# Performance work log

Hardware: AMD Instinct MI355X
Metric: run time of the kernel (lower is better)

## Reference

```python
import jax, jax.numpy as jnp
import numpy as np

DIM = 256
CODEBOOK_SIZE = 1024
CODEBOOK_DIM = 1024
COMMITMENT_COST = 1.0
CODEBOOK_COST = 0.25
LN_EPS = 1e-5


def setup_inputs() -> dict:
    key = jax.random.key(0)
    ks = jax.random.split(key, 6)
    x = jax.random.normal(ks[0], (4, 8192, DIM), dtype=jnp.float32)
    ln_gamma = jnp.ones((DIM,), jnp.float32)
    ln_beta = jnp.zeros((DIM,), jnp.float32)
    # pre_proj Linear(dim -> codebook_dim), stored as (in, out)
    pre_w = jax.random.normal(ks[1], (DIM, CODEBOOK_DIM), jnp.float32) / np.sqrt(DIM)
    pre_b = jnp.zeros((CODEBOOK_DIM,), jnp.float32)
    # codebook: unit-norm rows scaled by sqrt(codebook_dim)
    e = jax.random.normal(ks[2], (CODEBOOK_SIZE, CODEBOOK_DIM), jnp.float32)
    embed = e / jnp.linalg.norm(e, axis=1, keepdims=True) * np.sqrt(CODEBOOK_DIM)
    # post_proj Linear(codebook_dim -> dim)
    post_w = jax.random.normal(ks[3], (CODEBOOK_DIM, DIM), jnp.float32) / np.sqrt(CODEBOOK_DIM)
    post_b = jnp.zeros((DIM,), jnp.float32)
    return {"x": x, "ln_gamma": ln_gamma, "ln_beta": ln_beta,
            "pre_w": pre_w, "pre_b": pre_b, "embed": embed,
            "post_w": post_w, "post_b": post_b}


def _layer_norm(x, g, b):
    mu = jnp.mean(x, axis=-1, keepdims=True)
    var = jnp.mean(jnp.square(x - mu), axis=-1, keepdims=True)
    return (x - mu) * jax.lax.rsqrt(var + LN_EPS) * g + b


def reference(x, ln_gamma, ln_beta, pre_w, pre_b, embed, post_w, post_b):
    B, N, D = x.shape
    sg = jax.lax.stop_gradient
    # pre_norm -> GELU -> pre_proj
    x_normed = _layer_norm(x, ln_gamma, ln_beta)
    z_e = jax.nn.gelu(x_normed, approximate=False) @ pre_w + pre_b  # (B,N,Dc)
    flat = z_e.reshape(-1, CODEBOOK_DIM)  # (BN, Dc)
    # squared L2 distances to codebook: ||z||^2 - 2 z.E^T + ||e||^2
    z_sq = jnp.sum(flat * flat, axis=1, keepdims=True)        # (BN,1)
    e_sq = jnp.sum(embed * embed, axis=1)                      # (K,)
    dist = z_sq - 2.0 * (flat @ embed.T) + e_sq[None, :]       # (BN,K)
    indices = jnp.argmin(dist, axis=1)                          # (BN,)
    z_q = embed[indices]                                        # (BN,Dc)
    # losses
    codebook_loss = CODEBOOK_COST * jnp.mean(jnp.square(sg(flat) - z_q))
    commitment_loss = COMMITMENT_COST * jnp.mean(jnp.square(flat - sg(z_q)))
    vq_loss = codebook_loss + commitment_loss
    # straight-through estimator + post projection
    z_q_st = flat + sg(z_q - flat)
    quantized = (z_q_st.reshape(B, N, CODEBOOK_DIM)) @ post_w + post_b  # (B,N,D)
    return quantized, indices.reshape(B, N), vq_loss
```

## Files before the change

### kernel.cpp

```cpp
#include <hip/hip_runtime.h>
#include <math.h>

typedef __attribute__((ext_vector_type(8))) short short8;
typedef __attribute__((ext_vector_type(4))) float f32x4;

__device__ __forceinline__ unsigned short f2bf(float f) {
  unsigned u = __float_as_uint(f);
  unsigned r = (u + 0x7FFFu + ((u >> 16) & 1u)) >> 16;
  return (unsigned short)r;
}

__device__ __forceinline__ void gload_lds16(const void* gsrc, void* ldst) {
  __builtin_amdgcn_global_load_lds(
      (__attribute__((address_space(1))) void*)(void*)(size_t)(const char*)gsrc,
      (__attribute__((address_space(3))) void*)ldst, 16, 0, 0);
}

__global__ __launch_bounds__(256) void wtrans_kernel(
    const float* __restrict__ pre_w, float* __restrict__ wtf) {
  __shared__ float tile[64][65];
  const int bc = blockIdx.x;
  const int bd = blockIdx.y;
  const int t = threadIdx.x;
  const int col = t & 63, rr = t >> 6;
#pragma unroll
  for (int i = 0; i < 16; ++i) {
    int row = rr + i * 4;
    tile[row][col] = pre_w[(size_t)(bd * 64 + row) * 1024 + bc * 64 + col];
  }
  __syncthreads();
#pragma unroll
  for (int i = 0; i < 16; ++i) {
    int row = rr + i * 4;
    wtf[(size_t)(bc * 64 + row) * 256 + bd * 64 + col] = tile[col][row];
  }
}

__global__ __launch_bounds__(256) void esq_kernel(
    const float* __restrict__ embed, const float* __restrict__ pre_b,
    float* __restrict__ e_sq, float* __restrict__ qv, float* __restrict__ c0) {
  int t = threadIdx.x, l = t & 63, w = t >> 6;
  int k = blockIdx.x * 4 + w;
  const float* er = embed + (size_t)k * 1024;
  float s1 = 0.f, s2 = 0.f;
#pragma unroll
  for (int j = 0; j < 16; ++j) {
    float e = er[l + 64 * j];
    s1 += e * e;
    s2 += pre_b[l + 64 * j] * e;
  }
  for (int m = 32; m; m >>= 1) { s1 += __shfl_xor(s1, m); s2 += __shfl_xor(s2, m); }
  if (l == 0) { e_sq[k] = s1; qv[k] = s2; c0[k] = s1 - 2.0f * s2 - 1024.0f; }
}

__global__ __launch_bounds__(512) void pgemm_kernel(
    const float* __restrict__ embed, const float* __restrict__ wtf,
    float* __restrict__ prow, unsigned short* __restrict__ prowbf) {
  __shared__ float Es[4][1024];
  __shared__ double Pd[4][1024];
  const int t = threadIdx.x;
  const int k0 = blockIdx.x * 4;
  *(float4*)(&Es[0][0] + t * 8) = *(const float4*)(embed + (size_t)k0 * 1024 + t * 8);
  *(float4*)(&Es[0][0] + t * 8 + 4) = *(const float4*)(embed + (size_t)k0 * 1024 + t * 8 + 4);
  __syncthreads();
  const int sl = t >> 6;
  const int jg = t & 63;
  const int cbase = sl * 128;
  double a[4][4] = {};
  const float* wp = wtf + (size_t)cbase * 256 + jg * 4;
#pragma unroll 8
  for (int cc = 0; cc < 128; ++cc) {
    float4 w4 = *(const float4*)(wp + (size_t)cc * 256);
    int c = cbase + cc;
#pragma unroll
    for (int kk = 0; kk < 4; ++kk) {
      double e = (double)Es[kk][c];
      a[kk][0] += (double)w4.x * e;
      a[kk][1] += (double)w4.y * e;
      a[kk][2] += (double)w4.z * e;
      a[kk][3] += (double)w4.w * e;
    }
  }
  if (sl >= 4)
#pragma unroll
    for (int kk = 0; kk < 4; ++kk)
#pragma unroll
      for (int x = 0; x < 4; ++x) Pd[sl - 4][kk * 256 + jg * 4 + x] = a[kk][x];
  __syncthreads();
  if (sl < 4)
#pragma unroll
    for (int kk = 0; kk < 4; ++kk)
#pragma unroll
      for (int x = 0; x < 4; ++x) a[kk][x] += Pd[sl][kk * 256 + jg * 4 + x];
  __syncthreads();
  if (sl >= 2 && sl < 4)
#pragma unroll
    for (int kk = 0; kk < 4; ++kk)
#pragma unroll
      for (int x = 0; x < 4; ++x) Pd[sl - 2][kk * 256 + jg * 4 + x] = a[kk][x];
  __syncthreads();
  if (sl < 2)
#pragma unroll
    for (int kk = 0; kk < 4; ++kk)
#pragma unroll
      for (int x = 0; x < 4; ++x) a[kk][x] += Pd[sl][kk * 256 + jg * 4 + x];
  __syncthreads();
  if (sl == 1)
#pragma unroll
    for (int kk = 0; kk < 4; ++kk)
#pragma unroll
      for (int x = 0; x < 4; ++x) Pd[0][kk * 256 + jg * 4 + x] = a[kk][x];
  __syncthreads();
  if (sl == 0) {
#pragma unroll
    for (int kk = 0; kk < 4; ++kk) {
      float4 o;
      o.x = (float)(a[kk][0] + Pd[0][kk * 256 + jg * 4 + 0]);
      o.y = (float)(a[kk][1] + Pd[0][kk * 256 + jg * 4 + 1]);
      o.z = (float)(a[kk][2] + Pd[0][kk * 256 + jg * 4 + 2]);
      o.w = (float)(a[kk][3] + Pd[0][kk * 256 + jg * 4 + 3]);
      *(float4*)(prow + (size_t)(k0 + kk) * 256 + jg * 4) = o;
      ushort4 u;
      u.x = f2bf(o.x); u.y = f2bf(o.y); u.z = f2bf(o.z); u.w = f2bf(o.w);
      *(ushort4*)(prowbf + (size_t)(k0 + kk) * 256 + jg * 4) = u;
    }
  }
}

__global__ __launch_bounds__(512) void eproj_kernel(
    const float* __restrict__ embed, const float* __restrict__ post_w,
    const float* __restrict__ post_b, float* __restrict__ eproj) {
  __shared__ float Es[4][1024];
  __shared__ float Ps[8][1024];
  const int t = threadIdx.x;
  const int k0 = blockIdx.x * 4;
  *(float4*)(&Es[0][0] + t * 8) = *(const float4*)(embed + (size_t)k0 * 1024 + t * 8);
  *(float4*)(&Es[0][0] + t * 8 + 4) = *(const float4*)(embed + (size_t)k0 * 1024 + t * 8 + 4);
  __syncthreads();
  const int sl = t >> 6, jg = t & 63;
  const int dbase = sl * 128;
  float4 a[4] = {};
  const float* wp = post_w + (size_t)dbase * 256 + jg * 4;
#pragma unroll 8
  for (int dd = 0; dd < 128; ++dd) {
    float4 w4 = *(const float4*)(wp + (size_t)dd * 256);
    int d = dbase + dd;
#pragma unroll
    for (int kk = 0; kk < 4; ++kk) {
      float e = Es[kk][d];
      a[kk].x += w4.x * e; a[kk].y += w4.y * e;
      a[kk].z += w4.z * e; a[kk].w += w4.w * e;
    }
  }
#pragma unroll
  for (int kk = 0; kk < 4; ++kk)
    *(float4*)(&Ps[sl][kk * 256 + jg * 4]) = a[kk];
  __syncthreads();
#pragma unroll
  for (int rep = 0; rep < 2; ++rep) {
    int o = t + rep * 512;
    float s = Ps[0][o] + Ps[1][o] + Ps[2][o] + Ps[3][o] +
              Ps[4][o] + Ps[5][o] + Ps[6][o] + Ps[7][o];
    int kk = o >> 8, j = o & 255;
    eproj[(size_t)(k0 + kk) * 256 + j] = s + post_b[j];
  }
}

__global__ __launch_bounds__(512) void qmat_kernel(
    const float* __restrict__ pre_w, const float* __restrict__ wtf,
    const float* __restrict__ pre_b,
    unsigned short* __restrict__ qbf, float* __restrict__ wbv) {
  __shared__ float Es[4][1024];
  __shared__ float Ps[8][1024];
  const int t = threadIdx.x;
  const int sl = t >> 6, jg = t & 63;
  if (blockIdx.x < 64) {
    const int a0i = blockIdx.x * 4;
    *(float4*)(&Es[0][0] + t * 8) = *(const float4*)(pre_w + (size_t)a0i * 1024 + t * 8);
    *(float4*)(&Es[0][0] + t * 8 + 4) = *(const float4*)(pre_w + (size_t)a0i * 1024 + t * 8 + 4);
    __syncthreads();
    const int cbase = sl * 128;
    float4 a[4] = {};
    const float* wp = wtf + (size_t)cbase * 256 + jg * 4;
#pragma unroll 8
    for (int cc = 0; cc < 128; ++cc) {
      float4 w4 = *(const float4*)(wp + (size_t)cc * 256);
      int c = cbase + cc;
#pragma unroll
      for (int kk = 0; kk < 4; ++kk) {
        float e = Es[kk][c];
        a[kk].x += w4.x * e; a[kk].y += w4.y * e;
        a[kk].z += w4.z * e; a[kk].w += w4.w * e;
      }
    }
#pragma unroll
    for (int kk = 0; kk < 4; ++kk)
      *(float4*)(&Ps[sl][kk * 256 + jg * 4]) = a[kk];
    __syncthreads();
#pragma unroll
    for (int rep = 0; rep < 2; ++rep) {
      int o = t + rep * 512;
      float s = Ps[0][o] + Ps[1][o] + Ps[2][o] + Ps[3][o] +
                Ps[4][o] + Ps[5][o] + Ps[6][o] + Ps[7][o];
      int kk = o >> 8, j = o & 255;
      qbf[(size_t)(a0i + kk) * 256 + j] = f2bf(s);
    }
  } else {
    const int cbase = sl * 128;
    float4 a = {0.f, 0.f, 0.f, 0.f};
    const float* wp = wtf + (size_t)cbase * 256 + jg * 4;
#pragma unroll 8
    for (int cc = 0; cc < 128; ++cc) {
      float4 w4 = *(const float4*)(wp + (size_t)cc * 256);
      float b = pre_b[cbase + cc];
      a.x += w4.x * b; a.y += w4.y * b; a.z += w4.z * b; a.w += w4.w * b;
    }
    *(float4*)(&Ps[sl][jg * 4]) = a;
    float sb = 0.f;
    if (t < 256) {
      float4 bv = *(const float4*)(pre_b + t * 4);
      sb = bv.x * bv.x + bv.y * bv.y + bv.z * bv.z + bv.w * bv.w;
    }
    for (int m = 32; m; m >>= 1) sb += __shfl_xor(sb, m);
    if ((t & 63) == 0 && t < 256) Es[0][t >> 6] = sb;
    __syncthreads();
    if (t < 256) {
      float s = Ps[0][t] + Ps[1][t] + Ps[2][t] + Ps[3][t] +
                Ps[4][t] + Ps[5][t] + Ps[6][t] + Ps[7][t];
      wbv[t] = 2.f * s;
    }
    if (t == 0) wbv[256] = Es[0][0] + Es[0][1] + Es[0][2] + Es[0][3];
  }
}

__global__ __launch_bounds__(256) void lngelu_kernel(
    const float* __restrict__ x, const float* __restrict__ gamma,
    const float* __restrict__ beta, float* __restrict__ g,
    unsigned short* __restrict__ gbf) {
  int t = threadIdx.x, l = t & 63, w = t >> 6;
  int r = blockIdx.x * 4 + w;
  const float4 xv = *(const float4*)(x + (size_t)r * 256 + l * 4);
  float s = xv.x + xv.y + xv.z + xv.w;
  for (int m = 32; m; m >>= 1) s += __shfl_xor(s, m);
  const float mu = s * (1.0f / 256.0f);
  float dx = xv.x - mu, dy = xv.y - mu, dz = xv.z - mu, dw = xv.w - mu;
  float vs = dx * dx + dy * dy + dz * dz + dw * dw;
  for (int m = 32; m; m >>= 1) vs += __shfl_xor(vs, m);
  const float rstd = rsqrtf(vs * (1.0f / 256.0f) + 1e-5f);
  float4 gm = *(const float4*)(gamma + l * 4);
  float4 bt = *(const float4*)(beta + l * 4);
  float v0 = dx * rstd * gm.x + bt.x;
  float v1 = dy * rstd * gm.y + bt.y;
  float v2 = dz * rstd * gm.z + bt.z;
  float v3 = dw * rstd * gm.w + bt.w;
  const float is2 = 0.70710678118654752f;
  float4 o;
  o.x = 0.5f * v0 * (1.0f + erff(v0 * is2));
  o.y = 0.5f * v1 * (1.0f + erff(v1 * is2));
  o.z = 0.5f * v2 * (1.0f + erff(v2 * is2));
  o.w = 0.5f * v3 * (1.0f + erff(v3 * is2));
  *(float4*)(g + (size_t)r * 256 + l * 4) = o;
  ushort4 u;
  u.x = f2bf(o.x); u.y = f2bf(o.y); u.z = f2bf(o.z); u.w = f2bf(o.w);
  *(ushort4*)(gbf + (size_t)r * 256 + l * 4) = u;
}

__device__ __forceinline__ void stage_tile256(
    int t, const unsigned short* __restrict__ Asrc, size_t a_row_stride,
    const unsigned short* __restrict__ Bsrc, size_t b_row_stride, int k0,
    unsigned short* Ab, unsigned short* Bb) {
#pragma unroll
  for (int i = 0; i < 4; ++i) {
    int ca = t + 256 * i;
    int r = ca >> 3;
    int sp = (ca & 7) ^ (r & 7);
    gload_lds16(Asrc + (size_t)r * a_row_stride + k0 + sp * 8, (char*)Ab + ca * 16);
    gload_lds16(Bsrc + (size_t)r * b_row_stride + k0 + sp * 8, (char*)Bb + ca * 16);
  }
}

#define SAFE_LOOP_BODY(cur)                                                    \
    const unsigned short* Ab = &lds[cur][0];                                   \
    const unsigned short* Bb = &lds[cur][8192];                                \
    _Pragma("unroll")                                                          \
    for (int ks = 0; ks < 2; ++ks) {                                           \
      const int sp = ((ks << 2) + (l >> 4)) ^ (l & 7);                         \
      short8 af[4], bq[4];                                                     \
      _Pragma("unroll")                                                        \
      for (int mi = 0; mi < 4; ++mi)                                           \
        af[mi] = *(const short8*)(Ab + (wm + mi * 16 + (l & 15)) * 64 + sp * 8); \
      _Pragma("unroll")                                                        \
      for (int ni = 0; ni < 4; ++ni)                                           \
        bq[ni] = *(const short8*)(Bb + (wn + ni * 16 + (l & 15)) * 64 + sp * 8); \
      _Pragma("unroll")                                                        \
      for (int mi = 0; mi < 4; ++mi)                                           \
        _Pragma("unroll")                                                      \
        for (int ni = 0; ni < 4; ++ni)                                         \
          acc[mi][ni] = __builtin_amdgcn_mfma_f32_16x16x32_bf16(af[mi], bq[ni], acc[mi][ni], 0, 0, 0); \
    }

__global__ __launch_bounds__(256) void g1_kernel(
    const unsigned short* __restrict__ gbf,
    const unsigned short* __restrict__ prowbf,
    const float* __restrict__ c0,
    unsigned short* __restrict__ scores) {
  __shared__ unsigned short lds[2][16384];
  const int t = threadIdx.x;
  const int bn = blockIdx.x;
  const int bm = blockIdx.y;
  const int m0 = bm * 128;
  const unsigned short* Bsrc = prowbf + bn * 128 * 256;
  f32x4 acc[4][4] = {};
  const int w = t >> 6, l = t & 63;
  const int wm = (w >> 1) * 64, wn = (w & 1) * 64;

  stage_tile256(t, gbf + (size_t)m0 * 256, 256, Bsrc, 256, 0, &lds[0][0], &lds[0][8192]);
  __syncthreads();
  for (int kt = 0; kt < 4; ++kt) {
    const int cur = kt & 1;
    if (kt < 3)
      stage_tile256(t, gbf + (size_t)m0 * 256, 256, Bsrc, 256, (kt + 1) * 64,
                    &lds[cur ^ 1][0], &lds[cur ^ 1][8192]);
    SAFE_LOOP_BODY(cur)
    __syncthreads();
  }
  const int lrow = (l >> 4) * 4;
  const int lcol = l & 15;
  const int n0 = bn * 128;
#pragma unroll
  for (int mi = 0; mi < 4; ++mi)
#pragma unroll
    for (int ni = 0; ni < 4; ++ni) {
      int gcol = n0 + wn + ni * 16 + lcol;
      float cc = c0[gcol];
#pragma unroll
      for (int r = 0; r < 4; ++r) {
        int grow = m0 + wm + mi * 16 + lrow + r;
        scores[(size_t)grow * 1024 + gcol] = f2bf(cc - 2.0f * acc[mi][ni][r]);
      }
    }
}

__global__ __launch_bounds__(256) void zq_kernel(
    const unsigned short* __restrict__ gbf, const unsigned short* __restrict__ qbf,
    const float* __restrict__ g, const float* __restrict__ wbv,
    float* __restrict__ z_sq) {
  __shared__ unsigned short lds[2][16384];
  const int t = threadIdx.x;
  const int bn = blockIdx.x;
  const int bm = blockIdx.y;
  const int m0 = bm * 128;
  const unsigned short* Bsrc = qbf + bn * 128 * 256;
  f32x4 acc[4][4] = {};
  const int w = t >> 6, l = t & 63;
  const int wm = (w >> 1) * 64, wn = (w & 1) * 64;

  stage_tile256(t, gbf + (size_t)m0 * 256, 256, Bsrc, 256, 0, &lds[0][0], &lds[0][8192]);
  __syncthreads();
  for (int kt = 0; kt < 4; ++kt) {
    const int cur = kt & 1;
    if (kt < 3)
      stage_tile256(t, gbf + (size_t)m0 * 256, 256, Bsrc, 256, (kt + 1) * 64,
                    &lds[cur ^ 1][0], &lds[cur ^ 1][8192]);
    SAFE_LOOP_BODY(cur)
    __syncthreads();
  }
  const int lrow = (l >> 4) * 4;
  const int lcol = l & 15;
  const float bsq = wbv[256];
#pragma unroll
  for (int mi = 0; mi < 4; ++mi)
#pragma unroll
    for (int r = 0; r < 4; ++r) {
      int grow = m0 + wm + mi * 16 + lrow + r;
      float v = 0.f;
#pragma unroll
      for (int ni = 0; ni < 4; ++ni) {
        int gcol = bn * 128 + wn + ni * 16 + lcol;
        float gv = g[(size_t)grow * 256 + gcol];
        v += gv * (acc[mi][ni][r] + wbv[gcol]);
      }
      v += __shfl_xor(v, 1); v += __shfl_xor(v, 2);
      v += __shfl_xor(v, 4); v += __shfl_xor(v, 8);
      if (lcol == 0)
        atomicAdd(&z_sq[grow], v + ((bn == 0 && wn == 0) ? bsq : 0.f));
    }
}

__global__ __launch_bounds__(256) void refine_kernel(
    const unsigned short* __restrict__ scores, const float* __restrict__ g,
    const float* __restrict__ prow, const float* __restrict__ e_sq,
    const float* __restrict__ qv, const float* __restrict__ z_sq,
    const float* __restrict__ eproj, float* __restrict__ out_q,
    float* __restrict__ fidx, float* __restrict__ loss_slots) {
  const int t = threadIdx.x, l = t & 63, w = t >> 6;
  const int r = blockIdx.x * 4 + w;
  const unsigned short* srow = scores + (size_t)r * 1024;
  uint4 q0 = *(const uint4*)(srow + l * 16);
  uint4 q1 = *(const uint4*)(srow + l * 16 + 8);
  float f[16];
  {
    unsigned uu[8] = {q0.x, q0.y, q0.z, q0.w, q1.x, q1.y, q1.z, q1.w};
#pragma unroll
    for (int j = 0; j < 8; ++j) {
      f[2 * j] = __uint_as_float(uu[j] << 16);
      f[2 * j + 1] = __uint_as_float(uu[j] & 0xFFFF0000u);
    }
  }
  float mn = f[0];
#pragma unroll
  for (int j = 1; j < 16; ++j) mn = fminf(mn, f[j]);
  for (int m = 32; m; m >>= 1) mn = fminf(mn, __shfl_xor(mn, m));
  const float T = mn + 8.0f;

  float gv[4];
  const float* gr = g + (size_t)r * 256;
#pragma unroll
  for (int j = 0; j < 4; ++j) gv[j] = gr[l + 64 * j];

  float bestd = 1e30f; int bestk = 0x7fffffff;
#pragma unroll 1
  for (int j = 0; j < 16; ++j) {
    unsigned long long msk = __ballot(f[j] <= T);
    while (msk) {
      int src = __ffsll(msk) - 1;
      msk &= msk - 1;
      int k = src * 16 + j;
      const float* pr = prow + (size_t)k * 256;
      float p = 0.f;
#pragma unroll
      for (int jj = 0; jj < 4; ++jj) p += gv[jj] * pr[l + 64 * jj];
      for (int m = 32; m; m >>= 1) p += __shfl_xor(p, m);
      float d = e_sq[k] - 2.0f * (p + qv[k]);
      if (d < bestd || (d == bestd && k < bestk)) { bestd = d; bestk = k; }
    }
  }
  if (l == 0) {
    fidx[r] = (float)bestk;
    atomicAdd(&loss_slots[r & 2047], z_sq[r] + bestd);
  }
  float4 o = *(const float4*)(eproj + (size_t)bestk * 256 + l * 4);
  *(float4*)(out_q + (size_t)r * 256 + l * 4) = o;
}

__global__ __launch_bounds__(256) void loss_final_kernel(
    const float* __restrict__ slots, float* __restrict__ out_loss) {
  float s = 0.f;
  for (int i = threadIdx.x; i < 2048; i += 256) s += slots[i];
  for (int m = 32; m; m >>= 1) s += __shfl_xor(s, m);
  __shared__ float ws_[4];
  if ((threadIdx.x & 63) == 0) ws_[threadIdx.x >> 6] = s;
  __syncthreads();
  if (threadIdx.x == 0)
    out_loss[0] = 1.25f * (ws_[0] + ws_[1] + ws_[2] + ws_[3]) / 33554432.0f;
}

extern "C" void kernel_launch(void* const* d_in, const int* in_sizes, int n_in,
                              void* d_out, int out_size, void* d_ws, size_t ws_size,
                              hipStream_t stream) {
  const float* x = (const float*)d_in[0];
  const float* ln_g = (const float*)d_in[1];
  const float* ln_b = (const float*)d_in[2];
  const float* pre_w = (const float*)d_in[3];
  const float* pre_b = (const float*)d_in[4];
  const float* embed = (const float*)d_in[5];
  const float* post_w = (const float*)d_in[6];
  const float* post_b = (const float*)d_in[7];
  float* out_q = (float*)d_out;
  float* out_idx = out_q + 8388608;
  float* out_loss = out_q + 8421376;

  char* ws = (char*)d_ws;
  size_t off = 0;
  auto alloc = [&](size_t n) { char* p = ws + off; off += (n + 255) & ~(size_t)255; return p; };
  float* g_f32 = (float*)alloc(33554432);
  unsigned short* g_bf = (unsigned short*)alloc(16777216);
  unsigned short* scores = (unsigned short*)alloc(67108864);
  float* prow = (float*)alloc(1048576);
  unsigned short* prowbf = (unsigned short*)alloc(524288);
  unsigned short* qbf = (unsigned short*)alloc(131072);
  float* wtf = (float*)alloc(1048576);
  float* eproj = (float*)alloc(1048576);
  float* wbv = (float*)alloc(2048);
  float* e_sq = (float*)alloc(4096);
  float* qv = (float*)alloc(4096);
  float* c0 = (float*)alloc(4096);
  float* z_sq = (float*)alloc(131072);
  float* slots = (float*)alloc(8192);
  (void)ws_size; (void)in_sizes; (void)n_in; (void)out_size;

  hipMemsetAsync(z_sq, 0, 131072, stream);
  hipMemsetAsync(slots, 0, 8192, stream);

  dim3 wtg(16, 4);
  wtrans_kernel<<<wtg, 256, 0, stream>>>(pre_w, wtf);
  esq_kernel<<<256, 256, 0, stream>>>(embed, pre_b, e_sq, qv, c0);
  pgemm_kernel<<<256, 512, 0, stream>>>(embed, wtf, prow, prowbf);
  eproj_kernel<<<256, 512, 0, stream>>>(embed, post_w, post_b, eproj);
  qmat_kernel<<<65, 512, 0, stream>>>(pre_w, wtf, pre_b, qbf, wbv);
  lngelu_kernel<<<8192, 256, 0, stream>>>(x, ln_g, ln_b, g_f32, g_bf);
  dim3 g1grid(8, 256);
  g1_kernel<<<g1grid, 256, 0, stream>>>(g_bf, prowbf, c0, scores);
  dim3 zqgrid(2, 256);
  zq_kernel<<<zqgrid, 256, 0, stream>>>(g_bf, qbf, g_f32, wbv, z_sq);
  refine_kernel<<<8192, 256, 0, stream>>>(scores, g_f32, prow, e_sq, qv, z_sq,
                                          eproj, out_q, out_idx, slots);
  loss_final_kernel<<<1, 256, 0, stream>>>(slots, out_loss);
}
```

Baseline: 164.6 us.

## Merge six prep kernels into two block-dispatched kernels and swap GEMM grid axes

The transpose, e_sq, eproj and LayerNorm+GELU kernels are folded into one launch that picks its role from the block index, and pgemm and qmat are folded into a second launch. This cuts the number of small launches and the gaps between them, and lets independent prep work run concurrently. The g1 and zq grids now put the M dimension on blockIdx.x, which changes block scheduling order and so L2 reuse of the B operand. The cost is larger 48KB shared-memory reservations and 512-thread blocks for the light paths, which may lower occupancy for the LayerNorm blocks.

New measurement: 148.9 us. 1.11x faster.

```diff
diff --git a/kernel.cpp b/kernel.cpp
--- a/kernel.cpp
+++ b/kernel.cpp
@@ -16,166 +16,190 @@
       (__attribute__((address_space(3))) void*)ldst, 16, 0, 0);
 }
 
-__global__ __launch_bounds__(256) void wtrans_kernel(
-    const float* __restrict__ pre_w, float* __restrict__ wtf) {
-  __shared__ float tile[64][65];
-  const int bc = blockIdx.x;
-  const int bd = blockIdx.y;
+__global__ __launch_bounds__(512) void prep1_kernel(
+    const float* __restrict__ x, const float* __restrict__ ln_g,
+    const float* __restrict__ ln_b, const float* __restrict__ pre_w,
+    const float* __restrict__ pre_b, const float* __restrict__ embed,
+    const float* __restrict__ post_w, const float* __restrict__ post_b,
+    float* __restrict__ g, unsigned short* __restrict__ gbf,
+    float* __restrict__ wtf, float* __restrict__ e_sq,
+    float* __restrict__ qv, float* __restrict__ c0,
+    float* __restrict__ eproj) {
+  __shared__ __align__(16) char smem[49152];
+  const int blk = blockIdx.x;
   const int t = threadIdx.x;
-  const int col = t & 63, rr = t >> 6;
-#pragma unroll
-  for (int i = 0; i < 16; ++i) {
-    int row = rr + i * 4;
-    tile[row][col] = pre_w[(size_t)(bd * 64 + row) * 1024 + bc * 64 + col];
-  }
-  __syncthreads();
-#pragma unroll
-  for (int i = 0; i < 16; ++i) {
-    int row = rr + i * 4;
-    wtf[(size_t)(bc * 64 + row) * 256 + bd * 64 + col] = tile[col][row];
-  }
-}
-
-__global__ __launch_bounds__(256) void esq_kernel(
-    const float* __restrict__ embed, const float* __restrict__ pre_b,
-    float* __restrict__ e_sq, float* __restrict__ qv, float* __restrict__ c0) {
-  int t = threadIdx.x, l = t & 63, w = t >> 6;
-  int k = blockIdx.x * 4 + w;
-  const float* er = embed + (size_t)k * 1024;
-  float s1 = 0.f, s2 = 0.f;
-#pragma unroll
-  for (int j = 0; j < 16; ++j) {
-    float e = er[l + 64 * j];
-    s1 += e * e;
-    s2 += pre_b[l + 64 * j] * e;
-  }
-  for (int m = 32; m; m >>= 1) { s1 += __shfl_xor(s1, m); s2 += __shfl_xor(s2, m); }
-  if (l == 0) { e_sq[k] = s1; qv[k] = s2; c0[k] = s1 - 2.0f * s2 - 1024.0f; }
-}
-
-__global__ __launch_bounds__(512) void pgemm_kernel(
-    const float* __restrict__ embed, const float* __restrict__ wtf,
-    float* __restrict__ prow, unsigned short* __restrict__ prowbf) {
-  __shared__ float Es[4][1024];
-  __shared__ double Pd[4][1024];
-  const int t = threadIdx.x;
-  const int k0 = blockIdx.x * 4;
-  *(float4*)(&Es[0][0] + t * 8) = *(const float4*)(embed + (size_t)k0 * 1024 + t * 8);
-  *(float4*)(&Es[0][0] + t * 8 + 4) = *(const float4*)(embed + (size_t)k0 * 1024 + t * 8 + 4);
-  __syncthreads();
-  const int sl = t >> 6;
-  const int jg = t & 63;
-  const int cbase = sl * 128;
-  double a[4][4] = {};
-  const float* wp = wtf + (size_t)cbase * 256 + jg * 4;
+  if (blk < 4096) {
+    const int l = t & 63, w = t >> 6;
+    const int r = blk * 8 + w;
+    const float4 xv = *(const float4*)(x + (size_t)r * 256 + l * 4);
+    float s = xv.x + xv.y + xv.z + xv.w;
+    for (int m = 32; m; m >>= 1) s += __shfl_xor(s, m);
+    const float mu = s * (1.0f / 256.0f);
+    float dx = xv.x - mu, dy = xv.y - mu, dz = xv.z - mu, dw = xv.w - mu;
+    float vs = dx * dx + dy * dy + dz * dz + dw * dw;
+    for (int m = 32; m; m >>= 1) vs += __shfl_xor(vs, m);
+    const float rstd = rsqrtf(vs * (1.0f / 256.0f) + 1e-5f);
+    float4 gm = *(const float4*)(ln_g + l * 4);
+    float4 bt = *(const float4*)(ln_b + l * 4);
+    float v0 = dx * rstd * gm.x + bt.x;
+    float v1 = dy * rstd * gm.y + bt.y;
+    float v2 = dz * rstd * gm.z + bt.z;
+    float v3 = dw * rstd * gm.w + bt.w;
+    const float is2 = 0.70710678118654752f;
+    float4 o;
+    o.x = 0.5f * v0 * (1.0f + erff(v0 * is2));
+    o.y = 0.5f * v1 * (1.0f + erff(v1 * is2));
+    o.z = 0.5f * v2 * (1.0f + erff(v2 * is2));
+    o.w = 0.5f * v3 * (1.0f + erff(v3 * is2));
+    *(float4*)(g + (size_t)r * 256 + l * 4) = o;
+    ushort4 u;
+    u.x = f2bf(o.x); u.y = f2bf(o.y); u.z = f2bf(o.z); u.w = f2bf(o.w);
+    *(ushort4*)(gbf + (size_t)r * 256 + l * 4) = u;
+  } else if (blk < 4160) {
+    float (*tile)[65] = (float(*)[65])smem;
+    const int b = blk - 4096;
+    const int bc = b & 15, bd = b >> 4;
+    const int col = t & 63, rr = t >> 6;
+#pragma unroll
+    for (int i = 0; i < 8; ++i) {
+      int row = rr + i * 8;
+      tile[row][col] = pre_w[(size_t)(bd * 64 + row) * 1024 + bc * 64 + col];
+    }
+    __syncthreads();
+#pragma unroll
+    for (int i = 0; i < 8; ++i) {
+      int row = rr + i * 8;
+      wtf[(size_t)(bc * 64 + row) * 256 + bd * 64 + col] = tile[col][row];
+    }
+  } else if (blk < 4416) {
+    float (*Es)[1024] = (float(*)[1024])smem;
+    float (*Ps)[1024] = (float(*)[1024])(smem + 16384);
+    const int k0 = (blk - 4160) * 4;
+    *(float4*)(&Es[0][0] + t * 8) = *(const float4*)(embed + (size_t)k0 * 1024 + t * 8);
+    *(float4*)(&Es[0][0] + t * 8 + 4) = *(const float4*)(embed + (size_t)k0 * 1024 + t * 8 + 4);
+    __syncthreads();
+    const int sl = t >> 6, jg = t & 63;
+    const int dbase = sl * 128;
+    float4 a[4] = {};
+    const float* wp = post_w + (size_t)dbase * 256 + jg * 4;
 #pragma unroll 8
-  for (int cc = 0; cc < 128; ++cc) {
-    float4 w4 = *(const float4*)(wp + (size_t)cc * 256);
-    int c = cbase + cc;
-#pragma unroll
-    for (int kk = 0; kk < 4; ++kk) {
-      double e = (double)Es[kk][c];
-      a[kk][0] += (double)w4.x * e;
-      a[kk][1] += (double)w4.y * e;
-      a[kk][2] += (double)w4.z * e;
-      a[kk][3] += (double)w4.w * e;
-    }
-  }
-  if (sl >= 4)
+    for (int dd = 0; dd < 128; ++dd) {
+      float4 w4 = *(const float4*)(wp + (size_t)dd * 256);
+      int d = dbase + dd;
+#pragma unroll
+      for (int kk = 0; kk < 4; ++kk) {
+        float e = Es[kk][d];
+        a[kk].x += w4.x * e; a[kk].y += w4.y * e;
+        a[kk].z += w4.z * e; a[kk].w += w4.w * e;
+      }
+    }
 #pragma unroll
     for (int kk = 0; kk < 4; ++kk)
-#pragma unroll
-      for (int x = 0; x < 4; ++x) Pd[sl - 4][kk * 256 + jg * 4 + x] = a[kk][x];
-  __syncthreads();
-  if (sl < 4)
-#pragma unroll
-    for (int kk = 0; kk < 4; ++kk)
-#pragma unroll
-      for (int x = 0; x < 4; ++x) a[kk][x] += Pd[sl][kk * 256 + jg * 4 + x];
-  __syncthreads();
-  if (sl >= 2 && sl < 4)
-#pragma unroll
-    for (int kk = 0; kk < 4; ++kk)
-#pragma unroll
-      for (int x = 0; x < 4; ++x) Pd[sl - 2][kk * 256 + jg * 4 + x] = a[kk][x];
-  __syncthreads();
-  if (sl < 2)
-#pragma unroll
-    for (int kk = 0; kk < 4; ++kk)
-#pragma unroll
-      for (int x = 0; x < 4; ++x) a[kk][x] += Pd[sl][kk * 256 + jg * 4 + x];
-  __syncthreads();
-  if (sl == 1)
-#pragma unroll
-    for (int kk = 0; kk < 4; ++kk)
-#pragma unroll
-      for (int x = 0; x < 4; ++x) Pd[0][kk * 256 + jg * 4 + x] = a[kk][x];
-  __syncthreads();
-  if (sl == 0) {
-#pragma unroll
-    for (int kk = 0; kk < 4; ++kk) {
-      float4 o;
-      o.x = (float)(a[kk][0] + Pd[0][kk * 256 + jg * 4 + 0]);
-      o.y = (float)(a[kk][1] + Pd[0][kk * 256 + jg * 4 + 1]);
-      o.z = (float)(a[kk][2] + Pd[0][kk * 256 + jg * 4 + 2]);
-      o.w = (float)(a[kk][3] + Pd[0][kk * 256 + jg * 4 + 3]);
-      *(float4*)(prow + (size_t)(k0 + kk) * 256 + jg * 4) = o;
-      ushort4 u;
-      u.x = f2bf(o.x); u.y = f2bf(o.y); u.z = f2bf(o.z); u.w = f2bf(o.w);
-      *(ushort4*)(prowbf + (size_t)(k0 + kk) * 256 + jg * 4) = u;
-    }
-  }
-}
-
-__global__ __launch_bounds__(512) void eproj_kernel(
-    const float* __restrict__ embed, const float* __restrict__ post_w,
-    const float* __restrict__ post_b, float* __restrict__ eproj) {
-  __shared__ float Es[4][1024];
-  __shared__ float Ps[8][1024];
-  const int t = threadIdx.x;
-  const int k0 = blockIdx.x * 4;
-  *(float4*)(&Es[0][0] + t * 8) = *(const float4*)(embed + (size_t)k0 * 1024 + t * 8);
-  *(float4*)(&Es[0][0] + t * 8 + 4) = *(const float4*)(embed + (size_t)k0 * 1024 + t * 8 + 4);
-  __syncthreads();
-  const int sl = t >> 6, jg = t & 63;
-  const int dbase = sl * 128;
-  float4 a[4] = {};
-  const float* wp = post_w + (size_t)dbase * 256 + jg * 4;
-#pragma unroll 8
-  for (int dd = 0; dd < 128; ++dd) {
-    float4 w4 = *(const float4*)(wp + (size_t)dd * 256);
-    int d = dbase + dd;
-#pragma unroll
-    for (int kk = 0; kk < 4; ++kk) {
-      float e = Es[kk][d];
-      a[kk].x += w4.x * e; a[kk].y += w4.y * e;
-      a[kk].z += w4.z * e; a[kk].w += w4.w * e;
-    }
-  }
-#pragma unroll
-  for (int kk = 0; kk < 4; ++kk)
-    *(float4*)(&Ps[sl][kk * 256 + jg * 4]) = a[kk];
-  __syncthreads();
-#pragma unroll
-  for (int rep = 0; rep < 2; ++rep) {
-    int o = t + rep * 512;
-    float s = Ps[0][o] + Ps[1][o] + Ps[2][o] + Ps[3][o] +
-              Ps[4][o] + Ps[5][o] + Ps[6][o] + Ps[7][o];
-    int kk = o >> 8, j = o & 255;
-    eproj[(size_t)(k0 + kk) * 256 + j] = s + post_b[j];
-  }
-}
-
-__global__ __launch_bounds__(512) void qmat_kernel(
-    const float* __restrict__ pre_w, const float* __restrict__ wtf,
-    const float* __restrict__ pre_b,
+      *(float4*)(&Ps[sl][kk * 256 + jg * 4]) = a[kk];
+    __syncthreads();
+#pragma unroll
+    for (int rep = 0; rep < 2; ++rep) {
+      int o = t + rep * 512;
+      float s = Ps[0][o] + Ps[1][o] + Ps[2][o] + Ps[3][o] +
+                Ps[4][o] + Ps[5][o] + Ps[6][o] + Ps[7][o];
+      int kk = o >> 8, j = o & 255;
+      eproj[(size_t)(k0 + kk) * 256 + j] = s + post_b[j];
+    }
+  } else {
+    const int l = t & 63, w = t >> 6;
+    const int k = (blk - 4416) * 8 + w;
+    const float* er = embed + (size_t)k * 1024;
+    float s1 = 0.f, s2 = 0.f;
+#pragma unroll
+    for (int j = 0; j < 16; ++j) {
+      float e = er[l + 64 * j];
+      s1 += e * e;
+      s2 += pre_b[l + 64 * j] * e;
+    }
+    for (int m = 32; m; m >>= 1) { s1 += __shfl_xor(s1, m); s2 += __shfl_xor(s2, m); }
+    if (l == 0) { e_sq[k] = s1; qv[k] = s2; c0[k] = s1 - 2.0f * s2 - 1024.0f; }
+  }
+}
+
+__global__ __launch_bounds__(512) void prep2_kernel(
+    const float* __restrict__ embed, const float* __restrict__ pre_w,
+    const float* __restrict__ pre_b, const float* __restrict__ wtf,
+    float* __restrict__ prow, unsigned short* __restrict__ prowbf,
     unsigned short* __restrict__ qbf, float* __restrict__ wbv) {
-  __shared__ float Es[4][1024];
-  __shared__ float Ps[8][1024];
+  __shared__ __align__(16) char smem[49152];
   const int t = threadIdx.x;
   const int sl = t >> 6, jg = t & 63;
-  if (blockIdx.x < 64) {
-    const int a0i = blockIdx.x * 4;
+  if (blockIdx.x < 256) {
+    float (*Es)[1024] = (float(*)[1024])smem;
+    double (*Pd)[1024] = (double(*)[1024])(smem + 16384);
+    const int k0 = blockIdx.x * 4;
+    *(float4*)(&Es[0][0] + t * 8) = *(const float4*)(embed + (size_t)k0 * 1024 + t * 8);
+    *(float4*)(&Es[0][0] + t * 8 + 4) = *(const float4*)(embed + (size_t)k0 * 1024 + t * 8 + 4);
+    __syncthreads();
+    const int cbase = sl * 128;
+    double a[4][4] = {};
+    const float* wp = wtf + (size_t)cbase * 256 + jg * 4;
+#pragma unroll 8
+    for (int cc = 0; cc < 128; ++cc) {
+      float4 w4 = *(const float4*)(wp + (size_t)cc * 256);
+      int c = cbase + cc;
+#pragma unroll
+      for (int kk = 0; kk < 4; ++kk) {
+        double e = (double)Es[kk][c];
+        a[kk][0] += (double)w4.x * e;
+        a[kk][1] += (double)w4.y * e;
+        a[kk][2] += (double)w4.z * e;
+        a[kk][3] += (double)w4.w * e;
+      }
+    }
+    if (sl >= 4)
+#pragma unroll
+      for (int kk = 0; kk < 4; ++kk)
+#pragma unroll
+        for (int xx = 0; xx < 4; ++xx) Pd[sl - 4][kk * 256 + jg * 4 + xx] = a[kk][xx];
+    __syncthreads();
+    if (sl < 4)
+#pragma unroll
+      for (int kk = 0; kk < 4; ++kk)
+#pragma unroll
+        for (int xx = 0; xx < 4; ++xx) a[kk][xx] += Pd[sl][kk * 256 + jg * 4 + xx];
+    __syncthreads();
+    if (sl >= 2 && sl < 4)
+#pragma unroll
+      for (int kk = 0; kk < 4; ++kk)
+#pragma unroll
+        for (int xx = 0; xx < 4; ++xx) Pd[sl - 2][kk * 256 + jg * 4 + xx] = a[kk][xx];
+    __syncthreads();
+    if (sl < 2)
+#pragma unroll
+      for (int kk = 0; kk < 4; ++kk)
+#pragma unroll
+        for (int xx = 0; xx < 4; ++xx) a[kk][xx] += Pd[sl][kk * 256 + jg * 4 + xx];
+    __syncthreads();
+    if (sl == 1)
+#pragma unroll
+      for (int kk = 0; kk < 4; ++kk)
+#pragma unroll
+        for (int xx = 0; xx < 4; ++xx) Pd[0][kk * 256 + jg * 4 + xx] = a[kk][xx];
+    __syncthreads();
+    if (sl == 0) {
+#pragma unroll
+      for (int kk = 0; kk < 4; ++kk) {
+        float4 o;
+        o.x = (float)(a[kk][0] + Pd[0][kk * 256 + jg * 4 + 0]);
+        o.y = (float)(a[kk][1] + Pd[0][kk * 256 + jg * 4 + 1]);
+        o.z = (float)(a[kk][2] + Pd[0][kk * 256 + jg * 4 + 2]);
+        o.w = (float)(a[kk][3] + Pd[0][kk * 256 + jg * 4 + 3]);
+        *(float4*)(prow + (size_t)(k0 + kk) * 256 + jg * 4) = o;
+        ushort4 u;
+        u.x = f2bf(o.x); u.y = f2bf(o.y); u.z = f2bf(o.z); u.w = f2bf(o.w);
+        *(ushort4*)(prowbf + (size_t)(k0 + kk) * 256 + jg * 4) = u;
+      }
+    }
+  } else if (blockIdx.x < 320) {
+    float (*Es)[1024] = (float(*)[1024])smem;
+    float (*Ps)[1024] = (float(*)[1024])(smem + 16384);
+    const int a0i = (blockIdx.x - 256) * 4;
     *(float4*)(&Es[0][0] + t * 8) = *(const float4*)(pre_w + (size_t)a0i * 1024 + t * 8);
     *(float4*)(&Es[0][0] + t * 8 + 4) = *(const float4*)(pre_w + (size_t)a0i * 1024 + t * 8 + 4);
     __syncthreads();
@@ -206,6 +230,8 @@
       qbf[(size_t)(a0i + kk) * 256 + j] = f2bf(s);
     }
   } else {
+    float* Es0 = (float*)smem;
+    float (*Ps)[1024] = (float(*)[1024])(smem + 16384);
     const int cbase = sl * 128;
     float4 a = {0.f, 0.f, 0.f, 0.f};
     const float* wp = wtf + (size_t)cbase * 256 + jg * 4;
@@ -222,47 +248,15 @@
       sb = bv.x * bv.x + bv.y * bv.y + bv.z * bv.z + bv.w * bv.w;
     }
     for (int m = 32; m; m >>= 1) sb += __shfl_xor(sb, m);
-    if ((t & 63) == 0 && t < 256) Es[0][t >> 6] = sb;
+    if ((t & 63) == 0 && t < 256) Es0[t >> 6] = sb;
     __syncthreads();
     if (t < 256) {
       float s = Ps[0][t] + Ps[1][t] + Ps[2][t] + Ps[3][t] +
                 Ps[4][t] + Ps[5][t] + Ps[6][t] + Ps[7][t];
       wbv[t] = 2.f * s;
     }
-    if (t == 0) wbv[256] = Es[0][0] + Es[0][1] + Es[0][2] + Es[0][3];
-  }
-}
-
-__global__ __launch_bounds__(256) void lngelu_kernel(
-    const float* __restrict__ x, const float* __restrict__ gamma,
-    const float* __restrict__ beta, float* __restrict__ g,
-    unsigned short* __restrict__ gbf) {
-  int t = threadIdx.x, l = t & 63, w = t >> 6;
-  int r = blockIdx.x * 4 + w;
-  const float4 xv = *(const float4*)(x + (size_t)r * 256 + l * 4);
-  float s = xv.x + xv.y + xv.z + xv.w;
-  for (int m = 32; m; m >>= 1) s += __shfl_xor(s, m);
-  const float mu = s * (1.0f / 256.0f);
-  float dx = xv.x - mu, dy = xv.y - mu, dz = xv.z - mu, dw = xv.w - mu;
-  float vs = dx * dx + dy * dy + dz * dz + dw * dw;
-  for (int m = 32; m; m >>= 1) vs += __shfl_xor(vs, m);
-  const float rstd = rsqrtf(vs * (1.0f / 256.0f) + 1e-5f);
-  float4 gm = *(const float4*)(gamma + l * 4);
-  float4 bt = *(const float4*)(beta + l * 4);
-  float v0 = dx * rstd * gm.x + bt.x;
-  float v1 = dy * rstd * gm.y + bt.y;
-  float v2 = dz * rstd * gm.z + bt.z;
-  float v3 = dw * rstd * gm.w + bt.w;
-  const float is2 = 0.70710678118654752f;
-  float4 o;
-  o.x = 0.5f * v0 * (1.0f + erff(v0 * is2));
-  o.y = 0.5f * v1 * (1.0f + erff(v1 * is2));
-  o.z = 0.5f * v2 * (1.0f + erff(v2 * is2));
-  o.w = 0.5f * v3 * (1.0f + erff(v3 * is2));
-  *(float4*)(g + (size_t)r * 256 + l * 4) = o;
-  ushort4 u;
-  u.x = f2bf(o.x); u.y = f2bf(o.y); u.z = f2bf(o.z); u.w = f2bf(o.w);
-  *(ushort4*)(gbf + (size_t)r * 256 + l * 4) = u;
+    if (t == 0) wbv[256] = Es0[0] + Es0[1] + Es0[2] + Es0[3];
+  }
 }
 
 __device__ __forceinline__ void stage_tile256(
@@ -306,8 +300,8 @@
     unsigned short* __restrict__ scores) {
   __shared__ unsigned short lds[2][16384];
   const int t = threadIdx.x;
-  const int bn = blockIdx.x;
-  const int bm = blockIdx.y;
+  const int bm = blockIdx.x;
+  const int bn = blockIdx.y;
   const int m0 = bm * 128;
   const unsigned short* Bsrc = prowbf + bn * 128 * 256;
   f32x4 acc[4][4] = {};
@@ -347,8 +341,8 @@
     float* __restrict__ z_sq) {
   __shared__ unsigned short lds[2][16384];
   const int t = threadIdx.x;
-  const int bn = blockIdx.x;
-  const int bm = blockIdx.y;
+  const int bm = blockIdx.x;
+  const int bn = blockIdx.y;
   const int m0 = bm * 128;
   const unsigned short* Bsrc = qbf + bn * 128 * 256;
   f32x4 acc[4][4] = {};
@@ -492,16 +486,14 @@
   hipMemsetAsync(z_sq, 0, 131072, stream);
   hipMemsetAsync(slots, 0, 8192, stream);
 
-  dim3 wtg(16, 4);
-  wtrans_kernel<<<wtg, 256, 0, stream>>>(pre_w, wtf);
-  esq_kernel<<<256, 256, 0, stream>>>(embed, pre_b, e_sq, qv, c0);
-  pgemm_kernel<<<256, 512, 0, stream>>>(embed, wtf, prow, prowbf);
-  eproj_kernel<<<256, 512, 0, stream>>>(embed, post_w, post_b, eproj);
-  qmat_kernel<<<65, 512, 0, stream>>>(pre_w, wtf, pre_b, qbf, wbv);
-  lngelu_kernel<<<8192, 256, 0, stream>>>(x, ln_g, ln_b, g_f32, g_bf);
-  dim3 g1grid(8, 256);
+  prep1_kernel<<<4544, 512, 0, stream>>>(x, ln_g, ln_b, pre_w, pre_b, embed,
+                                         post_w, post_b, g_f32, g_bf, wtf,
+                                         e_sq, qv, c0, eproj);
+  prep2_kernel<<<321, 512, 0, stream>>>(embed, pre_w, pre_b, wtf, prow, prowbf,
+                                        qbf, wbv);
+  dim3 g1grid(256, 8);
   g1_kernel<<<g1grid, 256, 0, stream>>>(g_bf, prowbf, c0, scores);
-  dim3 zqgrid(2, 256);
+  dim3 zqgrid(256, 2);
   zq_kernel<<<zqgrid, 256, 0, stream>>>(g_bf, qbf, g_f32, wbv, z_sq);
   refine_kernel<<<8192, 256, 0, stream>>>(scores, g_f32, prow, e_sq, qv, z_sq,
                                           eproj, out_q, out_idx, slots);
```
